# Kernel optimization log

Hardware: AMD Instinct MI355X
Metric: run time of the kernel (lower is better)

The kernel has to match this reference:

```python
import jax, jax.numpy as jnp
import numpy as np

HEADS, FOLD_W, FOLD_H, PW, PH = 4, 2, 2, 2, 2


def setup_inputs() -> dict:
    key = jax.random.key(0)
    ks = jax.random.split(key, 4)
    B, C, W0, H0 = 64, 128, 56, 56
    hd = HEADS * 24  # 96
    return {
        "x": jax.random.normal(ks[0], (B, C, W0, H0), jnp.float32),
        "Wc": jax.random.normal(ks[1], (hd, C), jnp.float32) * 0.05,
        "bc": jnp.zeros((hd,), jnp.float32),
        "Wp": jax.random.normal(ks[2], (hd, C), jnp.float32) * 0.05,
        "bp": jnp.zeros((hd,), jnp.float32),
        "sim_alpha": jnp.ones((1,), jnp.float32),
        "sim_beta": jnp.zeros((1,), jnp.float32),
        "Wo": jax.random.normal(ks[3], (C, hd), jnp.float32) * 0.05,
        "bo": jnp.zeros((C,), jnp.float32),
    }


def _conv1x1(t, W, b):
    return jnp.einsum('oc,bcwh->bowh', W, t) + b[None, :, None, None]


def _forward(x, Wc, bc, Wp, bp, sim_alpha, sim_beta, Wo, bo):
    B, C, W0, H0 = x.shape
    value = _conv1x1(x, Wp, bp)   # [B, e*c, W0, H0]
    q = _conv1x1(x, Wc, bc)
    hd = q.shape[1] // HEADS
    # 'b (e c) w h -> (b e) c w h'
    split = lambda t: t.reshape(B * HEADS, hd, W0, H0)
    value, q = split(value), split(q)
    # fold: 'b c (f1 w) (f2 h) -> (b f1 f2) c w h'
    w2, h2 = W0 // FOLD_W, H0 // FOLD_H
    def fold(t):
        b0 = t.shape[0]
        return (t.reshape(b0, hd, FOLD_W, w2, FOLD_H, h2)
                 .transpose(0, 2, 4, 1, 3, 5)
                 .reshape(b0 * FOLD_W * FOLD_H, hd, w2, h2))
    value, q = fold(value), fold(q)
    b, c, w, h = q.shape
    # adaptive avg pool to (PW, PH): mean over equal blocks
    def adpool(t):
        return t.reshape(b, c, PW, w // PW, PH, h // PH).mean(axis=(3, 5))
    centers = adpool(q).reshape(b, c, PW * PH).transpose(0, 2, 1)          # [b, M, c]
    value_centers = adpool(value).reshape(b, c, PW * PH).transpose(0, 2, 1)
    qf = q.reshape(b, c, w * h).transpose(0, 2, 1)                          # [b, N, c]
    vf = value.reshape(b, c, w * h).transpose(0, 2, 1)
    eps = 1e-12
    cn = centers / jnp.clip(jnp.linalg.norm(centers, axis=-1, keepdims=True), eps)
    xn = qf / jnp.clip(jnp.linalg.norm(qf, axis=-1, keepdims=True), eps)
    sim = jax.nn.sigmoid(sim_beta + sim_alpha * jnp.einsum('bmc,bnc->bmn', cn, xn))  # [b, M, N]
    # hard top-1 assignment over centers axis
    idx = jnp.argmax(sim, axis=1)                                           # [b, N]
    mask = (jnp.arange(sim.shape[1])[None, :, None] == idx[:, None, :])
    sim = sim * mask
    # weighted combine (segment-sum over patches) instead of huge broadcast
    cluster = (jnp.einsum('bmn,bnc->bmc', sim, vf) + value_centers) / (sim.sum(-1, keepdims=True) + 1.0)
    patches = jnp.einsum('bmn,bmc->bnc', sim, cluster)                      # [b, N, c]
    patches = patches.transpose(0, 2, 1).reshape(b, c, w, h)
    # unfold: '(b f1 f2) c w h -> b c (f1 w) (f2 h)'
    patches = (patches.reshape(B * HEADS, FOLD_W, FOLD_H, c, w, h)
                      .transpose(0, 3, 1, 4, 2, 5)
                      .reshape(B * HEADS, c, W0, H0))
    patches = patches.reshape(B, HEADS * c, W0, H0)
    return _conv1x1(patches, Wo, bo)


def reference(x, Wc, bc, Wp, bp, sim_alpha, sim_beta, Wo, bo):
    return _forward(x, Wc, bc, Wp, bp, sim_alpha, sim_beta, Wo, bo)
```

## Files before the change

kernel.cpp:

```cpp
#include <hip/hip_runtime.h>
#include <math.h>

#define CIN 128
#define HD  96
#define SP  3136
#define ROW 56
#define SLAB 1568
#define YSTRIDE 9216

__global__ __launch_bounds__(256) void wtq_k(
    const float* __restrict__ Wc, float* __restrict__ Wt)
{
  const int idx = blockIdx.x * 256 + threadIdx.x;
  if (idx >= 96 * 128) return;
  const int o = idx >> 7, c = idx & 127;
  Wt[c * 96 + o] = Wc[idx];
}

__global__ __launch_bounds__(256) void pe_k(
    const float* __restrict__ Wo, const float* __restrict__ Wp,
    const float* __restrict__ bp, float* __restrict__ P, float* __restrict__ obp)
{
  const int e = blockIdx.x;
  __shared__ float ws[24][128];
  const int tid = threadIdx.x;
  for (int i = tid; i < 24 * 128; i += 256)
    ws[i >> 7][i & 127] = Wp[(size_t)(e * 24 + (i >> 7)) * CIN + (i & 127)];
  __syncthreads();
  const int co = tid & 127;
  const int cig = tid >> 7;
  float wo_r[24];
  #pragma unroll
  for (int c = 0; c < 24; ++c) wo_r[c] = Wo[(size_t)co * HD + e * 24 + c];
  for (int ci = cig * 64; ci < cig * 64 + 64; ++ci) {
    float s = 0.f;
    #pragma unroll
    for (int c = 0; c < 24; ++c) s = fmaf(wo_r[c], ws[c][ci], s);
    P[((size_t)e * 128 + ci) * 128 + co] = s;
  }
  if (cig == 0) {
    float s = 0.f;
    #pragma unroll
    for (int c = 0; c < 24; ++c) s = fmaf(wo_r[c], bp[e * 24 + c], s);
    obp[e * 128 + co] = s;
  }
}

__global__ __launch_bounds__(512) void q_conv(
    const float* __restrict__ x, const float* __restrict__ Wt,
    const float* __restrict__ bc, float* __restrict__ qbuf)
{
  const int st = blockIdx.x % 49;
  const int b  = blockIdx.x / 49;
  const float* xb = x + (size_t)b * CIN * SP + st * 64;

  __shared__ float xs[128][64];

  const int tid  = threadIdx.x;
  const int lane = tid & 63;
  const int o0   = __builtin_amdgcn_readfirstlane(tid >> 6) * 12;

  #pragma unroll
  for (int r = 0; r < 4; ++r) {
    const int i = tid + r * 512;
    const int cc = i >> 4, s4 = i & 15;
    float4 v = *reinterpret_cast<const float4*>(xb + (size_t)cc * SP + s4 * 4);
    *reinterpret_cast<float4*>(&xs[cc][s4 * 4]) = v;
  }
  __syncthreads();

  float acc[12];
  #pragma unroll
  for (int i = 0; i < 12; ++i) acc[i] = 0.f;

  #pragma unroll 4
  for (int c = 0; c < CIN; ++c) {
    const float* wr = Wt + (size_t)c * 96 + o0;
    const float4 w0 = *reinterpret_cast<const float4*>(wr + 0);
    const float4 w1 = *reinterpret_cast<const float4*>(wr + 4);
    const float4 w2 = *reinterpret_cast<const float4*>(wr + 8);
    const float xv = xs[c][lane];
    acc[0]  = fmaf(w0.x, xv, acc[0]);
    acc[1]  = fmaf(w0.y, xv, acc[1]);
    acc[2]  = fmaf(w0.z, xv, acc[2]);
    acc[3]  = fmaf(w0.w, xv, acc[3]);
    acc[4]  = fmaf(w1.x, xv, acc[4]);
    acc[5]  = fmaf(w1.y, xv, acc[5]);
    acc[6]  = fmaf(w1.z, xv, acc[6]);
    acc[7]  = fmaf(w1.w, xv, acc[7]);
    acc[8]  = fmaf(w2.x, xv, acc[8]);
    acc[9]  = fmaf(w2.y, xv, acc[9]);
    acc[10] = fmaf(w2.z, xv, acc[10]);
    acc[11] = fmaf(w2.w, xv, acc[11]);
  }
  #pragma unroll
  for (int i = 0; i < 12; ++i) {
    const int o = o0 + i;
    qbuf[((size_t)b * 96 + o) * SP + st * 64 + lane] = acc[i] + bc[o];
  }
}

__global__ __launch_bounds__(512, 4) void cluster_k(
    float* qbuf, const float* __restrict__ alpha_p, const float* __restrict__ beta_p)
{
  const int blk = blockIdx.x;
  const int f1  = blk & 1;
  const int be  = blk >> 1;
  const size_t base = (size_t)be * 24 * SP + (size_t)(f1 * 28) * ROW;
  float* qp = qbuf + base;

  __shared__ double cnd[24][8];
  __shared__ float  sbest[SLAB];
  __shared__ unsigned char ibest[SLAB];
  __shared__ float dnl[8];

  const int tid  = threadIdx.x;
  const int wid  = tid >> 6;
  const int lane = tid & 63;

  for (int c = wid; c < 24; c += 8) {
    const float* src = qp + (size_t)c * SP;
    double b0=0,b1=0,b2=0,b3=0,b4=0,b5=0,b6=0,b7=0;
    for (int n = lane; n < SLAB; n += 64) {
      const int w = n / 56, h = n - w * 56;
      const int hf = (h >= 28) ? (h - 28) : h;
      const int g  = ((h >= 28) ? 4 : 0) + ((w >= 14) ? 2 : 0) + ((hf >= 14) ? 1 : 0);
      const double val = (double)src[n];
      b0 += (g==0)?val:0.0; b1 += (g==1)?val:0.0;
      b2 += (g==2)?val:0.0; b3 += (g==3)?val:0.0;
      b4 += (g==4)?val:0.0; b5 += (g==5)?val:0.0;
      b6 += (g==6)?val:0.0; b7 += (g==7)?val:0.0;
    }
    #pragma unroll
    for (int m = 32; m >= 1; m >>= 1) {
      b0 += __shfl_xor(b0,m); b1 += __shfl_xor(b1,m);
      b2 += __shfl_xor(b2,m); b3 += __shfl_xor(b3,m);
      b4 += __shfl_xor(b4,m); b5 += __shfl_xor(b5,m);
      b6 += __shfl_xor(b6,m); b7 += __shfl_xor(b7,m);
    }
    if (lane == 0) {
      cnd[c][0]=b0*(1.0/196.0); cnd[c][1]=b1*(1.0/196.0);
      cnd[c][2]=b2*(1.0/196.0); cnd[c][3]=b3*(1.0/196.0);
      cnd[c][4]=b4*(1.0/196.0); cnd[c][5]=b5*(1.0/196.0);
      cnd[c][6]=b6*(1.0/196.0); cnd[c][7]=b7*(1.0/196.0);
    }
  }
  __syncthreads();
  if (tid < 8) {
    double s = 0.0;
    #pragma unroll
    for (int c = 0; c < 24; ++c) { double t = cnd[c][tid]; s += t * t; }
    const double inv = 1.0 / fmax(sqrt(s), 1e-12);
    #pragma unroll
    for (int c = 0; c < 24; ++c) cnd[c][tid] *= inv;
  }
  __syncthreads();

  const double alpha = (double)alpha_p[0];
  const double beta  = (double)beta_p[0];

  for (int n0 = tid; n0 < SLAB; n0 += 512) {
    const int h  = n0 % 56;
    const int gb = (h >= 28) ? 4 : 0;
    double z0=0,z1=0,z2=0,z3=0,nrm=0;
    for (int c = 0; c < 24; ++c) {
      const double qv = (double)qp[(size_t)c * SP + n0];
      z0 += cnd[c][gb+0]*qv; z1 += cnd[c][gb+1]*qv;
      z2 += cnd[c][gb+2]*qv; z3 += cnd[c][gb+3]*qv;
      nrm += qv*qv;
    }
    const double inv = 1.0 / fmax(sqrt(nrm), 1e-12);
    const double v0 = beta + alpha * (z0 * inv);
    const double v1 = beta + alpha * (z1 * inv);
    const double v2 = beta + alpha * (z2 * inv);
    const double v3 = beta + alpha * (z3 * inv);
    double zb = v0; int bi = 0;
    if (v1 > zb) { zb = v1; bi = 1; }
    if (v2 > zb) { zb = v2; bi = 2; }
    if (v3 > zb) { zb = v3; bi = 3; }
    sbest[n0] = (float)(1.0 / (1.0 + exp(-zb)));
    ibest[n0] = (unsigned char)(gb + bi);
  }
  __syncthreads();

  if (wid < 8) {
    float dn = 0.f;
    for (int ch = 0; ch < 25; ++ch) {
      const int n = ch * 64 + lane;
      const bool p = (n < SLAB) && (ibest[n] == (unsigned char)wid);
      dn += p ? sbest[n] : 0.f;
    }
    #pragma unroll
    for (int m = 32; m >= 1; m >>= 1) dn += __shfl_xor(dn, m);
    if (lane == 0) dnl[wid] = dn;
  }
  __syncthreads();

  for (int i = tid; i < SLAB; i += 512) {
    qp[i] = sbest[i];
    reinterpret_cast<unsigned int*>(qp + SP)[i] = (unsigned int)ibest[i];
  }
  if (tid < 8) qp[2 * (size_t)SP + tid] = dnl[tid];
}

__global__ __launch_bounds__(256, 2) void seg_k(
    float* qbuf, const float* __restrict__ x)
{
  const int bid = blockIdx.x;
  const int wh  = bid & 1;
  const int f2  = (bid >> 1) & 1;
  const int f1  = (bid >> 2) & 1;
  const int b   = bid >> 3;

  __shared__ float4 sq_l[392];
  __shared__ unsigned int gq_l[392];
  __shared__ float xT[56][130];
  __shared__ float ysum[16][128];
  __shared__ float xps[2][128];

  const int tid = threadIdx.x;
  const int c   = tid & 127;
  const int pg  = tid >> 7;

  for (int n = tid; n < 392; n += 256) {
    const int r = n / 28, hc = n - r * 28;
    const int n_slab = (wh * 14 + r) * 56 + f2 * 28 + hc;
    float4 s4; unsigned int gp = 0;
    #pragma unroll
    for (int e = 0; e < 4; ++e) {
      const float* qp = qbuf + (size_t)(b*4 + e) * 24 * SP + (size_t)(f1*28) * ROW;
      const float sv = qp[n_slab];
      const unsigned int gv = reinterpret_cast<const unsigned int*>(qp + SP)[n_slab];
      if (e==0) s4.x = sv; else if (e==1) s4.y = sv;
      else if (e==2) s4.z = sv; else s4.w = sv;
      gp |= (gv & 3u) << (2*e);
    }
    sq_l[n] = s4; gq_l[n] = gp;
  }

  float sa[16];
  #pragma unroll
  for (int i = 0; i < 16; ++i) sa[i] = 0.f;
  float xp0 = 0.f, xp1 = 0.f;

  const float* xb = x + (size_t)b * CIN * SP;
  const int rowbase = f1*28 + wh*14;

  for (int ch = 0; ch < 7; ++ch) {
    __syncthreads();
    #pragma unroll
    for (int k = 0; k < 7; ++k) {
      const int slot = tid + k * 256;
      const int c2 = slot / 14, p4 = slot - c2 * 14;
      const int rr = p4 / 7, col4 = p4 - rr * 7;
      const int w = rowbase + ch*2 + rr;
      const float4 v = *reinterpret_cast<const float4*>(
          xb + (size_t)c2 * SP + (size_t)w * ROW + f2*28 + col4*4);
      const int pxl = rr * 28 + col4 * 4;
      xT[pxl+0][c2] = v.x; xT[pxl+1][c2] = v.y;
      xT[pxl+2][c2] = v.z; xT[pxl+3][c2] = v.w;
    }
    __syncthreads();
    for (int i = 0; i < 28; ++i) {
      const int pxl = 2*i + pg;
      const int n   = ch*56 + pxl;
      const float4 s4 = sq_l[n];
      const int gp = __builtin_amdgcn_readfirstlane((int)gq_l[n]);
      const float xv = xT[pxl][c];
      {
        const int k = gp & 3;
        if      (k == 0) sa[0]  += s4.x * xv;
        else if (k == 1) sa[1]  += s4.x * xv;
        else if (k == 2) sa[2]  += s4.x * xv;
        else             sa[3]  += s4.x * xv;
      }
      {
        const int k = (gp >> 2) & 3;
        if      (k == 0) sa[4]  += s4.y * xv;
        else if (k == 1) sa[5]  += s4.y * xv;
        else if (k == 2) sa[6]  += s4.y * xv;
        else             sa[7]  += s4.y * xv;
      }
      {
        const int k = (gp >> 4) & 3;
        if      (k == 0) sa[8]  += s4.z * xv;
        else if (k == 1) sa[9]  += s4.z * xv;
        else if (k == 2) sa[10] += s4.z * xv;
        else             sa[11] += s4.z * xv;
      }
      {
        const int k = (gp >> 6) & 3;
        if      (k == 0) sa[12] += s4.w * xv;
        else if (k == 1) sa[13] += s4.w * xv;
        else if (k == 2) sa[14] += s4.w * xv;
        else             sa[15] += s4.w * xv;
      }
      const int hc = (pxl >= 28) ? (pxl - 28) : pxl;
      if (hc >= 14) xp1 += xv; else xp0 += xv;
    }
  }

  __syncthreads();
  if (pg == 0) {
    #pragma unroll
    for (int k = 0; k < 16; ++k) ysum[k][c] = sa[k];
    xps[0][c] = xp0; xps[1][c] = xp1;
  }
  __syncthreads();
  if (pg == 1) {
    #pragma unroll
    for (int k = 0; k < 16; ++k) ysum[k][c] += sa[k];
    xps[0][c] += xp0; xps[1][c] += xp1;
  }
  __syncthreads();

  float* ybase = qbuf + ((size_t)b*96 + 9) * SP + (size_t)f1 * YSTRIDE;
  for (int i = tid; i < 16*128; i += 256) {
    const int row = i >> 7, cc = i & 127;
    ybase[((wh*2 + f2)*16 + row)*128 + cc] = ysum[row][cc];
  }
  {
    const int hb = tid >> 7, cc = tid & 127;
    ybase[64*128 + (f2*4 + wh*2 + hb)*128 + cc] = xps[hb][cc];
  }
}

__global__ __launch_bounds__(256) void proj_k(
    float* qbuf, const float* __restrict__ P, const float* __restrict__ obp)
{
  const int bid = blockIdx.x;
  const int b = bid >> 1, f1 = bid & 1;
  __shared__ float ylds[32][128];
  __shared__ float invs[32];
  const int tid = threadIdx.x;

  if (tid < 32) {
    const int e = tid >> 3, g = tid & 7;
    const float* dnp = qbuf + ((size_t)(b*4 + e) * 24 + 2) * SP + (size_t)(f1*28) * ROW;
    invs[tid] = 1.f / (dnp[g] + 1.f);
  }
  __syncthreads();

  const float* yp = qbuf + ((size_t)b*96 + 9) * SP + (size_t)f1 * YSTRIDE;
  for (int i = tid; i < 32*128; i += 256) {
    const int eg = i >> 7, cc = i & 127;
    const int e = eg >> 3, g = eg & 7, ff2 = g >> 2, m = g & 3;
    const float v = yp[((0 + ff2)*16 + e*4 + m)*128 + cc]
                  + yp[((2 + ff2)*16 + e*4 + m)*128 + cc]
                  + yp[64*128 + g*128 + cc] * (1.f/196.f);
    ylds[eg][cc] = v * invs[eg];
  }
  __syncthreads();

  const int co = tid & 127;
  const int e0 = (tid >> 7) * 2;
  float a0[8], a1[8];
  const float o0 = obp[e0 * 128 + co], o1 = obp[(e0 + 1) * 128 + co];
  #pragma unroll
  for (int g = 0; g < 8; ++g) { a0[g] = o0; a1[g] = o1; }
  for (int ci = 0; ci < 128; ++ci) {
    const float p0 = P[((size_t)e0 * 128 + ci) * 128 + co];
    const float p1 = P[((size_t)(e0 + 1) * 128 + ci) * 128 + co];
    #pragma unroll
    for (int g = 0; g < 8; ++g) {
      a0[g] = fmaf(p0, ylds[e0 * 8 + g][ci], a0[g]);
      a1[g] = fmaf(p1, ylds[(e0 + 1) * 8 + g][ci], a1[g]);
    }
  }
  float* pout = qbuf + ((size_t)b * 96 + 3 + f1 * 3) * SP;
  #pragma unroll
  for (int g = 0; g < 8; ++g) {
    pout[(e0 * 8 + g) * 128 + co]       = a0[g];
    pout[((e0 + 1) * 8 + g) * 128 + co] = a1[g];
  }
}

__global__ __launch_bounds__(256) void out_k(
    const float* __restrict__ qbuf, const float* __restrict__ bo,
    float* __restrict__ out)
{
  const int bid = blockIdx.x;
  const int b   = bid / 28;
  const int rem = bid % 28;
  const int f1  = rem / 14;
  const int rp  = rem % 14;
  const int n0  = rp * 112;

  __shared__ float  proj_l[4096];
  __shared__ float4 s_l4[112];
  __shared__ unsigned int g_l[112];
  __shared__ float  out_l[56 * 132];

  const int tid = threadIdx.x;

  {
    const float4* pg = reinterpret_cast<const float4*>(
        qbuf + ((size_t)b * 96 + 3 + f1*3) * SP);
    float4* pl = reinterpret_cast<float4*>(proj_l);
    #pragma unroll
    for (int r = 0; r < 4; ++r) pl[tid + r * 256] = pg[tid + r * 256];
  }
  for (int i = tid; i < 112; i += 256) {
    float4 sv; unsigned int gp = 0;
    #pragma unroll
    for (int e = 0; e < 4; ++e) {
      const float* sp = qbuf + ((size_t)(b*4 + e) * 24) * SP + (size_t)(f1*28) * ROW;
      const float sval = sp[n0 + i];
      const unsigned int gv = reinterpret_cast<const unsigned int*>(sp + SP)[n0 + i];
      if (e == 0) sv.x = sval; else if (e == 1) sv.y = sval;
      else if (e == 2) sv.z = sval; else sv.w = sval;
      gp |= (gv & 7u) << (8 * e);
    }
    s_l4[i] = sv; g_l[i] = gp;
  }
  __syncthreads();

  const int cq  = tid & 31;
  const int sub = tid >> 5;
  const float4 bo4 = *reinterpret_cast<const float4*>(bo + cq * 4);
  const float4* pl4 = reinterpret_cast<const float4*>(proj_l);

  for (int chunk = 0; chunk < 2; ++chunk) {
    const int pbase = chunk * 56;
    #pragma unroll
    for (int i = 0; i < 7; ++i) {
      const int pxl = sub * 7 + i;
      const int px  = pbase + pxl;
      const float4 sv = s_l4[px];
      const unsigned int gp = g_l[px];
      float4 acc = bo4;
      {
        const float4 p = pl4[(0*8 + (gp        & 7u)) * 32 + cq];
        acc.x = fmaf(sv.x, p.x, acc.x); acc.y = fmaf(sv.x, p.y, acc.y);
        acc.z = fmaf(sv.x, p.z, acc.z); acc.w = fmaf(sv.x, p.w, acc.w);
      }
      {
        const float4 p = pl4[(1*8 + ((gp >> 8) & 7u)) * 32 + cq];
        acc.x = fmaf(sv.y, p.x, acc.x); acc.y = fmaf(sv.y, p.y, acc.y);
        acc.z = fmaf(sv.y, p.z, acc.z); acc.w = fmaf(sv.y, p.w, acc.w);
      }
      {
        const float4 p = pl4[(2*8 + ((gp >> 16) & 7u)) * 32 + cq];
        acc.x = fmaf(sv.z, p.x, acc.x); acc.y = fmaf(sv.z, p.y, acc.y);
        acc.z = fmaf(sv.z, p.z, acc.z); acc.w = fmaf(sv.z, p.w, acc.w);
      }
      {
        const float4 p = pl4[(3*8 + ((gp >> 24) & 7u)) * 32 + cq];
        acc.x = fmaf(sv.w, p.x, acc.x); acc.y = fmaf(sv.w, p.y, acc.y);
        acc.z = fmaf(sv.w, p.z, acc.z); acc.w = fmaf(sv.w, p.w, acc.w);
      }
      *reinterpret_cast<float4*>(&out_l[pxl * 132 + cq * 4]) = acc;
    }
    __syncthreads();
    for (int t = tid; t < 128 * 56; t += 256) {
      const int co = t / 56, pxl = t - co * 56;
      out[((size_t)b * 128 + co) * SP + (size_t)f1 * SLAB + n0 + pbase + pxl] =
          out_l[pxl * 132 + co];
    }
    __syncthreads();
  }
}

extern "C" void kernel_launch(void* const* d_in, const int* in_sizes, int n_in,
                              void* d_out, int out_size, void* d_ws, size_t ws_size,
                              hipStream_t stream) {
  const float* x  = (const float*)d_in[0];
  const float* Wc = (const float*)d_in[1];
  const float* bc = (const float*)d_in[2];
  const float* Wp = (const float*)d_in[3];
  const float* bp = (const float*)d_in[4];
  const float* sa = (const float*)d_in[5];
  const float* sb = (const float*)d_in[6];
  const float* Wo = (const float*)d_in[7];
  const float* bo = (const float*)d_in[8];
  float* out  = (float*)d_out;
  float* qbuf = (float*)d_ws;
  float* Pbuf = out;
  float* obpb = out + 65536;
  float* Wtq  = out + 66048;

  wtq_k    <<<dim3(48),      dim3(256), 0, stream>>>(Wc, Wtq);
  pe_k     <<<dim3(4),       dim3(256), 0, stream>>>(Wo, Wp, bp, Pbuf, obpb);
  q_conv   <<<dim3(64 * 49), dim3(512), 0, stream>>>(x, Wtq, bc, qbuf);
  cluster_k<<<dim3(512),     dim3(512), 0, stream>>>(qbuf, sa, sb);
  seg_k    <<<dim3(512),     dim3(256), 0, stream>>>(qbuf, x);
  proj_k   <<<dim3(128),     dim3(256), 0, stream>>>(qbuf, Pbuf, obpb);
  out_k    <<<dim3(1792),    dim3(256), 0, stream>>>(qbuf, bo, out);
}
```

Measured before the change: 224.6 us.

## Stage q slab through LDS once and fuse center pooling with similarity accumulation

cluster_k now loads the q slab into shared memory in three chunks of 8 channels with float4 copies. Each chunk is used both for the center pooling and for the per-pixel dot products, so the second global read of q goes away. Center normalization is folded in as a per-center scale applied at the end instead of being written back into cnd. The block grows to 768 threads so each thread owns at most three pixels. The change adds about 50KB of LDS and extra barriers, which may reduce occupancy.

```diff
diff --git a/kernel.cpp b/kernel.cpp
--- a/kernel.cpp
+++ b/kernel.cpp
@@ -100,7 +100,7 @@
   }
 }
 
-__global__ __launch_bounds__(512, 4) void cluster_k(
+__global__ __launch_bounds__(768, 2) void cluster_k(
     float* qbuf, const float* __restrict__ alpha_p, const float* __restrict__ beta_p)
 {
   const int blk = blockIdx.x;
@@ -109,77 +109,148 @@
   const size_t base = (size_t)be * 24 * SP + (size_t)(f1 * 28) * ROW;
   float* qp = qbuf + base;
 
+  __shared__ float  qs[8][SLAB];
   __shared__ double cnd[24][8];
+  __shared__ double invg[8];
   __shared__ float  sbest[SLAB];
   __shared__ unsigned char ibest[SLAB];
-  __shared__ float dnl[8];
+  __shared__ float  dnl[8];
 
   const int tid  = threadIdx.x;
   const int wid  = tid >> 6;
   const int lane = tid & 63;
 
-  for (int c = wid; c < 24; c += 8) {
-    const float* src = qp + (size_t)c * SP;
-    double b0=0,b1=0,b2=0,b3=0,b4=0,b5=0,b6=0,b7=0;
-    for (int n = lane; n < SLAB; n += 64) {
-      const int w = n / 56, h = n - w * 56;
-      const int hf = (h >= 28) ? (h - 28) : h;
-      const int g  = ((h >= 28) ? 4 : 0) + ((w >= 14) ? 2 : 0) + ((hf >= 14) ? 1 : 0);
-      const double val = (double)src[n];
-      b0 += (g==0)?val:0.0; b1 += (g==1)?val:0.0;
-      b2 += (g==2)?val:0.0; b3 += (g==3)?val:0.0;
-      b4 += (g==4)?val:0.0; b5 += (g==5)?val:0.0;
-      b6 += (g==6)?val:0.0; b7 += (g==7)?val:0.0;
-    }
-    #pragma unroll
-    for (int m = 32; m >= 1; m >>= 1) {
-      b0 += __shfl_xor(b0,m); b1 += __shfl_xor(b1,m);
-      b2 += __shfl_xor(b2,m); b3 += __shfl_xor(b3,m);
-      b4 += __shfl_xor(b4,m); b5 += __shfl_xor(b5,m);
-      b6 += __shfl_xor(b6,m); b7 += __shfl_xor(b7,m);
-    }
-    if (lane == 0) {
-      cnd[c][0]=b0*(1.0/196.0); cnd[c][1]=b1*(1.0/196.0);
-      cnd[c][2]=b2*(1.0/196.0); cnd[c][3]=b3*(1.0/196.0);
-      cnd[c][4]=b4*(1.0/196.0); cnd[c][5]=b5*(1.0/196.0);
-      cnd[c][6]=b6*(1.0/196.0); cnd[c][7]=b7*(1.0/196.0);
+  const int p0 = tid, p1 = tid + 768, p2 = tid + 1536;
+  const bool has2 = (tid < 32);
+  const bool hb0 = (p0 % 56) >= 28;
+  const bool hb1 = (p1 % 56) >= 28;
+  const bool hb2 = has2 ? ((p2 % 56) >= 28) : false;
+
+  double z00=0,z01=0,z02=0,z03=0;
+  double z10=0,z11=0,z12=0,z13=0;
+  double z20=0,z21=0,z22=0,z23=0;
+  double nq0=0, nq1=0, nq2=0;
+
+  for (int ck = 0; ck < 3; ++ck) {
+    __syncthreads();
+    for (int i = tid; i < 3136; i += 768) {
+      const int cc = i / 392, s4 = i - cc * 392;
+      float4 v = *reinterpret_cast<const float4*>(qp + (size_t)(ck*8 + cc) * SP + s4*4);
+      *reinterpret_cast<float4*>(&qs[cc][s4*4]) = v;
+    }
+    __syncthreads();
+    if (wid < 8) {
+      double b0=0,b1=0,b2=0,b3=0,b4=0,b5=0,b6=0,b7=0;
+      for (int n = lane; n < SLAB; n += 64) {
+        const int w = n / 56, h = n - w * 56;
+        const int hf = (h >= 28) ? (h - 28) : h;
+        const int g  = ((h >= 28) ? 4 : 0) + ((w >= 14) ? 2 : 0) + ((hf >= 14) ? 1 : 0);
+        const double val = (double)qs[wid][n];
+        b0 += (g==0)?val:0.0; b1 += (g==1)?val:0.0;
+        b2 += (g==2)?val:0.0; b3 += (g==3)?val:0.0;
+        b4 += (g==4)?val:0.0; b5 += (g==5)?val:0.0;
+        b6 += (g==6)?val:0.0; b7 += (g==7)?val:0.0;
+      }
+      #pragma unroll
+      for (int m = 32; m >= 1; m >>= 1) {
+        b0 += __shfl_xor(b0,m); b1 += __shfl_xor(b1,m);
+        b2 += __shfl_xor(b2,m); b3 += __shfl_xor(b3,m);
+        b4 += __shfl_xor(b4,m); b5 += __shfl_xor(b5,m);
+        b6 += __shfl_xor(b6,m); b7 += __shfl_xor(b7,m);
+      }
+      if (lane == 0) {
+        const int c = ck*8 + wid;
+        cnd[c][0]=b0*(1.0/196.0); cnd[c][1]=b1*(1.0/196.0);
+        cnd[c][2]=b2*(1.0/196.0); cnd[c][3]=b3*(1.0/196.0);
+        cnd[c][4]=b4*(1.0/196.0); cnd[c][5]=b5*(1.0/196.0);
+        cnd[c][6]=b6*(1.0/196.0); cnd[c][7]=b7*(1.0/196.0);
+      }
+    }
+    __syncthreads();
+    #pragma unroll
+    for (int u = 0; u < 8; ++u) {
+      const int c = ck*8 + u;
+      const double cd0 = cnd[c][0], cd1 = cnd[c][1], cd2 = cnd[c][2], cd3 = cnd[c][3];
+      const double cd4 = cnd[c][4], cd5 = cnd[c][5], cd6 = cnd[c][6], cd7 = cnd[c][7];
+      {
+        const double qv = (double)qs[u][p0];
+        z00 += (hb0 ? cd4 : cd0) * qv;
+        z01 += (hb0 ? cd5 : cd1) * qv;
+        z02 += (hb0 ? cd6 : cd2) * qv;
+        z03 += (hb0 ? cd7 : cd3) * qv;
+        nq0 += qv * qv;
+      }
+      {
+        const double qv = (double)qs[u][p1];
+        z10 += (hb1 ? cd4 : cd0) * qv;
+        z11 += (hb1 ? cd5 : cd1) * qv;
+        z12 += (hb1 ? cd6 : cd2) * qv;
+        z13 += (hb1 ? cd7 : cd3) * qv;
+        nq1 += qv * qv;
+      }
+      if (has2) {
+        const double qv = (double)qs[u][p2];
+        z20 += (hb2 ? cd4 : cd0) * qv;
+        z21 += (hb2 ? cd5 : cd1) * qv;
+        z22 += (hb2 ? cd6 : cd2) * qv;
+        z23 += (hb2 ? cd7 : cd3) * qv;
+        nq2 += qv * qv;
+      }
     }
   }
   __syncthreads();
   if (tid < 8) {
     double s = 0.0;
     #pragma unroll
-    for (int c = 0; c < 24; ++c) { double t = cnd[c][tid]; s += t * t; }
-    const double inv = 1.0 / fmax(sqrt(s), 1e-12);
-    #pragma unroll
-    for (int c = 0; c < 24; ++c) cnd[c][tid] *= inv;
+    for (int c = 0; c < 24; ++c) { const double t = cnd[c][tid]; s += t * t; }
+    invg[tid] = 1.0 / fmax(sqrt(s), 1e-12);
   }
   __syncthreads();
 
   const double alpha = (double)alpha_p[0];
   const double beta  = (double)beta_p[0];
 
-  for (int n0 = tid; n0 < SLAB; n0 += 512) {
-    const int h  = n0 % 56;
-    const int gb = (h >= 28) ? 4 : 0;
-    double z0=0,z1=0,z2=0,z3=0,nrm=0;
-    for (int c = 0; c < 24; ++c) {
-      const double qv = (double)qp[(size_t)c * SP + n0];
-      z0 += cnd[c][gb+0]*qv; z1 += cnd[c][gb+1]*qv;
-      z2 += cnd[c][gb+2]*qv; z3 += cnd[c][gb+3]*qv;
-      nrm += qv*qv;
-    }
-    const double inv = 1.0 / fmax(sqrt(nrm), 1e-12);
-    const double v0 = beta + alpha * (z0 * inv);
-    const double v1 = beta + alpha * (z1 * inv);
-    const double v2 = beta + alpha * (z2 * inv);
-    const double v3 = beta + alpha * (z3 * inv);
+  {
+    const int gB = hb0 ? 4 : 0;
+    const double inv = 1.0 / fmax(sqrt(nq0), 1e-12);
+    const double v0 = beta + alpha * (z00 * invg[gB+0] * inv);
+    const double v1 = beta + alpha * (z01 * invg[gB+1] * inv);
+    const double v2 = beta + alpha * (z02 * invg[gB+2] * inv);
+    const double v3 = beta + alpha * (z03 * invg[gB+3] * inv);
     double zb = v0; int bi = 0;
     if (v1 > zb) { zb = v1; bi = 1; }
     if (v2 > zb) { zb = v2; bi = 2; }
     if (v3 > zb) { zb = v3; bi = 3; }
-    sbest[n0] = (float)(1.0 / (1.0 + exp(-zb)));
-    ibest[n0] = (unsigned char)(gb + bi);
+    sbest[p0] = (float)(1.0 / (1.0 + exp(-zb)));
+    ibest[p0] = (unsigned char)(gB + bi);
+  }
+  {
+    const int gB = hb1 ? 4 : 0;
+    const double inv = 1.0 / fmax(sqrt(nq1), 1e-12);
+    const double v0 = beta + alpha * (z10 * invg[gB+0] * inv);
+    const double v1 = beta + alpha * (z11 * invg[gB+1] * inv);
+    const double v2 = beta + alpha * (z12 * invg[gB+2] * inv);
+    const double v3 = beta + alpha * (z13 * invg[gB+3] * inv);
+    double zb = v0; int bi = 0;
+    if (v1 > zb) { zb = v1; bi = 1; }
+    if (v2 > zb) { zb = v2; bi = 2; }
+    if (v3 > zb) { zb = v3; bi = 3; }
+    sbest[p1] = (float)(1.0 / (1.0 + exp(-zb)));
+    ibest[p1] = (unsigned char)(gB + bi);
+  }
+  if (has2) {
+    const int gB = hb2 ? 4 : 0;
+    const double inv = 1.0 / fmax(sqrt(nq2), 1e-12);
+    const double v0 = beta + alpha * (z20 * invg[gB+0] * inv);
+    const double v1 = beta + alpha * (z21 * invg[gB+1] * inv);
+    const double v2 = beta + alpha * (z22 * invg[gB+2] * inv);
+    const double v3 = beta + alpha * (z23 * invg[gB+3] * inv);
+    double zb = v0; int bi = 0;
+    if (v1 > zb) { zb = v1; bi = 1; }
+    if (v2 > zb) { zb = v2; bi = 2; }
+    if (v3 > zb) { zb = v3; bi = 3; }
+    sbest[p2] = (float)(1.0 / (1.0 + exp(-zb)));
+    ibest[p2] = (unsigned char)(gB + bi);
   }
   __syncthreads();
 
@@ -196,7 +267,7 @@
   }
   __syncthreads();
 
-  for (int i = tid; i < SLAB; i += 512) {
+  for (int i = tid; i < SLAB; i += 768) {
     qp[i] = sbest[i];
     reinterpret_cast<unsigned int*>(qp + SP)[i] = (unsigned int)ibest[i];
   }
@@ -482,7 +553,7 @@
   wtq_k    <<<dim3(48),      dim3(256), 0, stream>>>(Wc, Wtq);
   pe_k     <<<dim3(4),       dim3(256), 0, stream>>>(Wo, Wp, bp, Pbuf, obpb);
   q_conv   <<<dim3(64 * 49), dim3(512), 0, stream>>>(x, Wtq, bc, qbuf);
-  cluster_k<<<dim3(512),     dim3(512), 0, stream>>>(qbuf, sa, sb);
+  cluster_k<<<dim3(512),     dim3(768), 0, stream>>>(qbuf, sa, sb);
   seg_k    <<<dim3(512),     dim3(256), 0, stream>>>(qbuf, x);
   proj_k   <<<dim3(128),     dim3(256), 0, stream>>>(qbuf, Pbuf, obpb);
   out_k    <<<dim3(1792),    dim3(256), 0, stream>>>(qbuf, bo, out);
```

Result: slower. 280.9 us (+25.1%).
